# Performance work log

Measured on AMD Instinct MI355X. Metric: run time of the kernel, lower is better.

## Reference

```python
import jax, jax.numpy as jnp
import numpy as np

# --- Instant-NGP hashgrid config (from INGP.build_encoding) ---
L = 16            # cfg_model.encoding.levels
F = 2             # cfg_model.encoding.hashgrid.dim
T = 1 << 19       # 2 ** log2_hashmap_size
BASE = 16         # 2 ** min_logres
FINEST = 2048     # 2 ** max_logres
GROWTH = np.exp((np.log(FINEST) - np.log(BASE)) / (L - 1))
RES = np.floor(BASE * GROWTH ** np.arange(L)).astype(np.float32)  # per-level resolution
VMIN, VMAX = -1.0, 1.0  # voxel_range
N_POINTS = 524288

# 8 trilinear corner offsets, and NGP spatial-hash primes
CORNERS = np.array([[i, j, k] for i in (0, 1) for j in (0, 1) for k in (0, 1)],
                   dtype=np.uint32)                       # [8,3]
PRIMES = np.array([1, 2654435761, 805459861], dtype=np.uint32)


def setup_inputs() -> dict:
    key = jax.random.key(0)
    k1, k2 = jax.random.split(key)
    points_3D = jax.random.uniform(k1, (N_POINTS, 3), minval=-1.0, maxval=1.0,
                                   dtype=jnp.float32)
    # torch-ngp 'uniform' init: U(-1e-4, 1e-4)
    tables = jax.random.uniform(k2, (L, T, F), minval=-1e-4, maxval=1e-4,
                                dtype=jnp.float32)
    return {"points_3D": points_3D, "tables": tables}


def _hash_encode(x, tables):
    """x: [N,3] in [0,1]; tables: [L,T,F] -> [N, L*F]."""
    corners_u = jnp.asarray(CORNERS)            # [8,3] uint32
    corners_b = jnp.asarray(CORNERS.astype(bool))
    p0u, p1u, p2u = (jnp.uint32(int(p)) for p in PRIMES)
    mask = jnp.uint32(T - 1)

    def level(table, r):
        pos = x * r                              # [N,3]
        p0 = jnp.floor(pos)
        w = pos - p0                             # trilinear weights [N,3]
        c = p0.astype(jnp.uint32)[:, None, :] + corners_u[None]  # [N,8,3]
        h = (c[..., 0] * p0u) ^ (c[..., 1] * p1u) ^ (c[..., 2] * p2u)
        idx = (h & mask).astype(jnp.int32)       # [N,8] hashed bucket ids
        vals = table[idx]                        # [N,8,F] irregular gather
        wc = jnp.where(corners_b[None], w[:, None, :], 1.0 - w[:, None, :]).prod(-1)
        return jnp.einsum('nc,ncf->nf', wc, vals)  # [N,F]

    feats = jax.vmap(level)(tables, jnp.asarray(RES))  # [L,N,F]
    n = x.shape[0]
    return jnp.transpose(feats, (1, 0, 2)).reshape(n, L * F)


def reference(points_3D, tables):
    # _encode_3D with contract=False: normalize to [0,1] over voxel_range
    x = (points_3D - VMIN) / (VMAX - VMIN)
    feat = _hash_encode(x, tables)
    return feat.astype(jnp.float32)
```

## Files before the change

kernel.cpp:

```cpp
#include <hip/hip_runtime.h>
#include <cmath>


constexpr int LVLS = 16;
constexpr unsigned TBL = 1u << 19;
constexpr unsigned TMASK = TBL - 1u;
constexpr unsigned P1 = 2654435761u;
constexpr unsigned P2 = 805459861u;
constexpr int NBINS = 32768;
constexpr int CAP = 24;
constexpr int MAIN = NBINS * CAP;
constexpr int OVCAP = 65536;
constexpr int S_TOT = MAIN + OVCAP;
constexpr int SLOTS_PER_FINE_BLOCK = 512;

typedef float vf2 __attribute__((ext_vector_type(2)));
typedef float vf4 __attribute__((ext_vector_type(4)));

struct ResArr { float r[LVLS]; };

__device__ __forceinline__ unsigned spread5(unsigned v) {
    v &= 31u;
    v = (v | (v << 8)) & 0x100Fu;
    v = (v | (v << 4)) & 0x10C3u;
    v = (v | (v << 2)) & 0x1249u;
    return v;
}

__device__ __forceinline__ unsigned bin_key(float px, float py, float pz) {
    float x = (px + 1.0f) * 0.5f;
    float y = (py + 1.0f) * 0.5f;
    float z = (pz + 1.0f) * 0.5f;
    unsigned bx = (unsigned)fminf(31.f, fmaxf(0.f, floorf(x * 32.f)));
    unsigned by = (unsigned)fminf(31.f, fmaxf(0.f, floorf(y * 32.f)));
    unsigned bz = (unsigned)fminf(31.f, fmaxf(0.f, floorf(z * 32.f)));
    return spread5(bx) | (spread5(by) << 1) | (spread5(bz) << 2);
}

__device__ __forceinline__ void level_gather(
    const float2* __restrict__ tab, float r,
    float x, float y, float z, float& f0, float& f1)
{
    float posx = x * r, posy = y * r, posz = z * r;
    float fx = floorf(posx), fy = floorf(posy), fz = floorf(posz);
    float wx = posx - fx, wy = posy - fy, wz = posz - fz;
    unsigned ix = (unsigned)fx, iy = (unsigned)fy, iz = (unsigned)fz;
    unsigned hx0 = ix, hx1 = ix + 1u;
    unsigned hy0 = iy * P1;
    unsigned hz0 = iz * P2, hz1 = hz0 + P2;

    unsigned hyz[4];
    hyz[0] = hy0 ^ hz0;
    hyz[1] = hy0 ^ hz1;
    hyz[2] = (hy0 + P1) ^ hz0;
    hyz[3] = (hy0 + P1) ^ hz1;

    float2 v[8];
    if ((ix & 1u) == 0u) {
        #pragma unroll
        for (int yz = 0; yz < 4; ++yz) {
            unsigned b0 = (hx0 ^ hyz[yz]) & TMASK;
            vf4 qd = *(const vf4*)(tab + (b0 & ~1u));
            float2 lo = make_float2(qd.x, qd.y);
            float2 hi = make_float2(qd.z, qd.w);
            bool odd = (b0 & 1u) != 0u;
            v[yz]     = odd ? hi : lo;
            v[4 + yz] = odd ? lo : hi;
        }
    } else {
        #pragma unroll
        for (int yz = 0; yz < 4; ++yz) {
            unsigned b0 = (hx0 ^ hyz[yz]) & TMASK;
            unsigned b1 = (hx1 ^ hyz[yz]) & TMASK;
            v[yz]     = tab[b0];
            v[4 + yz] = tab[b1];
        }
    }

    float ox = 1.0f - wx, oy = 1.0f - wy, oz = 1.0f - wz;
    float w[8];
    w[0] = (ox * oy) * oz;
    w[1] = (ox * oy) * wz;
    w[2] = (ox * wy) * oz;
    w[3] = (ox * wy) * wz;
    w[4] = (wx * oy) * oz;
    w[5] = (wx * oy) * wz;
    w[6] = (wx * wy) * oz;
    w[7] = (wx * wy) * wz;

    f0 = w[0] * v[0].x;
    f1 = w[0] * v[0].y;
    #pragma unroll
    for (int c = 1; c < 8; ++c) {
        f0 += w[c] * v[c].x;
        f1 += w[c] * v[c].y;
    }
}

__device__ __forceinline__ void encode_point_direct(
    const float* __restrict__ tables, const ResArr& ra,
    float px, float py, float pz, vf4* __restrict__ row)
{
    float x = (px + 1.0f) * 0.5f;
    float y = (py + 1.0f) * 0.5f;
    float z = (pz + 1.0f) * 0.5f;
    float acc[2 * LVLS];
    #pragma unroll
    for (int l = 0; l < LVLS; ++l) {
        const float2* __restrict__ tab = (const float2*)tables + (size_t)l * TBL;
        float f0, f1;
        level_gather(tab, ra.r[l], x, y, z, f0, f1);
        acc[2 * l] = f0; acc[2 * l + 1] = f1;
    }
    #pragma unroll
    for (int k = 0; k < 8; ++k) {
        vf4 o;
        o.x = acc[4 * k + 0]; o.y = acc[4 * k + 1];
        o.z = acc[4 * k + 2]; o.w = acc[4 * k + 3];
        __builtin_nontemporal_store(o, row + k);
    }
}

__global__ __launch_bounds__(256) void ingp_scatter1(
    const float* __restrict__ pts, unsigned* __restrict__ cnt,
    vf4* __restrict__ slots, const float* __restrict__ tables,
    vf4* __restrict__ out, ResArr ra, int npts)
{
    int i = blockIdx.x * 256 + threadIdx.x;
    if (i >= npts) return;
    float px = pts[i * 3 + 0], py = pts[i * 3 + 1], pz = pts[i * 3 + 2];
    unsigned bin = bin_key(px, py, pz);
    unsigned pos = atomicAdd(&cnt[bin], 1u);
    vf4 o; o.x = px; o.y = py; o.z = pz; o.w = __int_as_float(i);
    if (pos < (unsigned)CAP) {
        __builtin_nontemporal_store(o, slots + (size_t)bin * CAP + pos);
    } else {
        unsigned ov = atomicAdd(&cnt[NBINS], 1u);
        if (ov < (unsigned)OVCAP) {
            __builtin_nontemporal_store(o, slots + MAIN + ov);
        } else {
            encode_point_direct(tables, ra, px, py, pz,
                                out + (size_t)i * 8);
        }
    }
}

__device__ __forceinline__ bool slot_valid(
    const unsigned* __restrict__ cnt, int sidx)
{
    if (sidx < MAIN) {
        unsigned bin = (unsigned)sidx / (unsigned)CAP;
        unsigned within = (unsigned)sidx - bin * (unsigned)CAP;
        unsigned c = cnt[bin];
        return within < (c < (unsigned)CAP ? c : (unsigned)CAP);
    } else {
        unsigned idx = (unsigned)(sidx - MAIN);
        unsigned c = cnt[NBINS];
        return idx < (c < (unsigned)OVCAP ? c : (unsigned)OVCAP);
    }
}

__global__ __launch_bounds__(256) void ingp_fine(
    const vf4* __restrict__ slots, const unsigned* __restrict__ cnt,
    const float* __restrict__ tables,
    float2* __restrict__ ws,
    ResArr ra)
{
    int b = blockIdx.x;
    int lvl = 8 + (b & 7);
    int q = b >> 3;
    int t = threadIdx.x;

    float r = ra.r[lvl];
    const float2* __restrict__ tab = (const float2*)tables + (size_t)lvl * TBL;
    float2* __restrict__ wrow = ws + (size_t)(lvl - 8) * S_TOT;

    #pragma unroll
    for (int s = 0; s < 2; ++s) {
        int sidx = q * SLOTS_PER_FINE_BLOCK + t + s * 256;
        if (!slot_valid(cnt, sidx)) continue;
        vf4 v = slots[sidx];
        float x = (v.x + 1.0f) * 0.5f;
        float y = (v.y + 1.0f) * 0.5f;
        float z = (v.z + 1.0f) * 0.5f;
        float f0, f1;
        level_gather(tab, r, x, y, z, f0, f1);
        vf2 o; o.x = f0; o.y = f1;
        __builtin_nontemporal_store(o, (vf2*)(wrow + sidx));
    }
}

__global__ __launch_bounds__(256) void ingp_finish(
    const vf4* __restrict__ slots, const unsigned* __restrict__ cnt,
    const float* __restrict__ tables,
    const float2* __restrict__ ws,
    vf4* __restrict__ out,
    ResArr ra)
{
    __shared__ float2 a[LVLS][258];
    __shared__ int s_orig[256];
    int base = blockIdx.x * 256;
    int t = threadIdx.x;
    int sidx = base + t;

    bool valid = slot_valid(cnt, sidx);
    float px = -1.0f, py = -1.0f, pz = -1.0f;
    int orig = -1;
    if (valid) {
        vf4 v4 = slots[sidx];
        px = v4.x; py = v4.y; pz = v4.z;
        orig = __float_as_int(v4.w);
    }
    s_orig[t] = orig;
    float x = (px + 1.0f) * 0.5f;
    float y = (py + 1.0f) * 0.5f;
    float z = (pz + 1.0f) * 0.5f;

    #pragma unroll
    for (int l = 0; l < 8; ++l) {
        const float2* __restrict__ tab = (const float2*)tables + (size_t)l * TBL;
        float f0, f1;
        level_gather(tab, ra.r[l], x, y, z, f0, f1);
        a[l][t] = make_float2(f0, f1);
    }
    #pragma unroll
    for (int l = 8; l < LVLS; ++l) {
        vf2 w = __builtin_nontemporal_load(
            (const vf2*)(ws + (size_t)(l - 8) * S_TOT + sidx));
        a[l][t] = make_float2(w.x, w.y);
    }
    __syncthreads();

    int j = t & 7;
    int pl = t >> 3;
    #pragma unroll
    for (int it = 0; it < 8; ++it) {
        int pt = pl + it * 32;
        int og = s_orig[pt];
        if (og >= 0) {
            float2 u = a[2 * j][pt];
            float2 v = a[2 * j + 1][pt];
            vf4 o; o.x = u.x; o.y = u.y; o.z = v.x; o.w = v.y;
            __builtin_nontemporal_store(o, (vf4*)(out + (size_t)og * 8 + j));
        }
    }
}

__global__ __launch_bounds__(256) void ingp_fused_raw(
    const float* __restrict__ pts,
    const float* __restrict__ tables,
    vf4* __restrict__ out, ResArr ra, int npts)
{
    int i = blockIdx.x * 256 + threadIdx.x;
    if (i >= npts) return;
    encode_point_direct(tables, ra,
                        pts[i * 3 + 0], pts[i * 3 + 1], pts[i * 3 + 2],
                        out + (size_t)i * 8);
}

extern "C" void kernel_launch(void* const* d_in, const int* in_sizes, int n_in,
                              void* d_out, int out_size, void* d_ws, size_t ws_size,
                              hipStream_t stream) {
    const float* pts    = (const float*)d_in[0];
    const float* tables = (const float*)d_in[1];
    int npts = in_sizes[0] / 3;

    ResArr ra;
    double growth = exp((log(2048.0) - log(16.0)) / 15.0);
    for (int l = 0; l < LVLS; ++l)
        ra.r[l] = (float)floor(16.0 * pow(growth, (double)l));

    int pgrid = (npts + 255) / 256;

    size_t fine_bytes = 8ull * S_TOT * sizeof(float2);
    size_t slot_bytes = (size_t)S_TOT * sizeof(vf4);
    size_t cnt_bytes  = (NBINS + 1) * sizeof(unsigned);
    size_t need = fine_bytes + slot_bytes + cnt_bytes;

    if (ws_size >= need) {
        char* w = (char*)d_ws;
        float2*   wsf   = (float2*)w;        w += fine_bytes;
        vf4*      slots = (vf4*)w;           w += slot_bytes;
        unsigned* cnt   = (unsigned*)w;

        hipMemsetAsync(cnt, 0, cnt_bytes, stream);
        hipLaunchKernelGGL(ingp_scatter1, dim3(pgrid), dim3(256), 0, stream,
                           pts, cnt, slots, tables, (vf4*)d_out, ra, npts);
        hipLaunchKernelGGL(ingp_fine,
                           dim3(8 * (S_TOT / SLOTS_PER_FINE_BLOCK)), dim3(256),
                           0, stream, slots, cnt, tables, wsf, ra);
        hipLaunchKernelGGL(ingp_finish, dim3(S_TOT / 256), dim3(256), 0, stream,
                           slots, cnt, tables, wsf, (vf4*)d_out, ra);
    } else {
        hipLaunchKernelGGL(ingp_fused_raw, dim3(pgrid), dim3(256), 0, stream,
                           pts, tables, (vf4*)d_out, ra, npts);
    }
}
```

Before: 309.3 us.

## Fold coarse-level gathers into the fine kernel and slim the finish pass

Moves the coarse levels 0-7 gather work out of the finish kernel and into the fine-level kernel. Every fifth group of blocks handles coarse levels for 256 slots and writes output features 0-15 directly, so coarse and fine gathers run concurrently in one launch. The finish kernel now only copies the eight fine-level results from the workspace into output columns 16-31. Bin capacity drops from 24 to 20 to shrink the slot array, at the risk of more overflow into the shared overflow region. Slot reads now use nontemporal loads.

Result: slower. 348.1 us (+12.5%).

```diff
diff --git a/kernel.cpp b/kernel.cpp
--- a/kernel.cpp
+++ b/kernel.cpp
@@ -8,11 +8,13 @@
 constexpr unsigned P1 = 2654435761u;
 constexpr unsigned P2 = 805459861u;
 constexpr int NBINS = 32768;
-constexpr int CAP = 24;
+constexpr int CAP = 20;
 constexpr int MAIN = NBINS * CAP;
 constexpr int OVCAP = 65536;
 constexpr int S_TOT = MAIN + OVCAP;
-constexpr int SLOTS_PER_FINE_BLOCK = 512;
+constexpr int NFINE = S_TOT / 512;
+constexpr int NCOARSE = S_TOT / 256;
+constexpr int T_OCT = NFINE + NCOARSE / 8;
 
 typedef float vf2 __attribute__((ext_vector_type(2)));
 typedef float vf4 __attribute__((ext_vector_type(4)));
@@ -160,88 +162,115 @@
     }
 }
 
-__global__ __launch_bounds__(256) void ingp_fine(
+__global__ __launch_bounds__(256) void ingp_fuse(
     const vf4* __restrict__ slots, const unsigned* __restrict__ cnt,
     const float* __restrict__ tables,
     float2* __restrict__ ws,
+    vf4* __restrict__ out,
     ResArr ra)
 {
+    __shared__ float2 a[8][258];
+    __shared__ int s_orig[256];
     int b = blockIdx.x;
-    int lvl = 8 + (b & 7);
-    int q = b >> 3;
+    int oct = b >> 3, l8 = b & 7;
     int t = threadIdx.x;
 
-    float r = ra.r[lvl];
-    const float2* __restrict__ tab = (const float2*)tables + (size_t)lvl * TBL;
-    float2* __restrict__ wrow = ws + (size_t)(lvl - 8) * S_TOT;
-
-    #pragma unroll
-    for (int s = 0; s < 2; ++s) {
-        int sidx = q * SLOTS_PER_FINE_BLOCK + t + s * 256;
-        if (!slot_valid(cnt, sidx)) continue;
-        vf4 v = slots[sidx];
-        float x = (v.x + 1.0f) * 0.5f;
-        float y = (v.y + 1.0f) * 0.5f;
-        float z = (v.z + 1.0f) * 0.5f;
-        float f0, f1;
-        level_gather(tab, r, x, y, z, f0, f1);
-        vf2 o; o.x = f0; o.y = f1;
-        __builtin_nontemporal_store(o, (vf2*)(wrow + sidx));
+    if (oct % 5 == 4) {
+        int c = (oct / 5) * 8 + l8;
+        int sidx = c * 256 + t;
+        bool valid = slot_valid(cnt, sidx);
+        float px = -1.0f, py = -1.0f, pz = -1.0f;
+        int orig = -1;
+        if (valid) {
+            vf4 v = __builtin_nontemporal_load(slots + sidx);
+            px = v.x; py = v.y; pz = v.z; orig = __float_as_int(v.w);
+        }
+        s_orig[t] = orig;
+        float x = (px + 1.0f) * 0.5f;
+        float y = (py + 1.0f) * 0.5f;
+        float z = (pz + 1.0f) * 0.5f;
+        #pragma unroll
+        for (int l = 0; l < 8; ++l) {
+            const float2* __restrict__ tab =
+                (const float2*)tables + (size_t)l * TBL;
+            float f0, f1;
+            level_gather(tab, ra.r[l], x, y, z, f0, f1);
+            a[l][t] = make_float2(f0, f1);
+        }
+        __syncthreads();
+        int j = t & 3, sl = t >> 2;
+        #pragma unroll
+        for (int it = 0; it < 4; ++it) {
+            int s = sl + it * 64;
+            int og = s_orig[s];
+            if (og >= 0) {
+                float2 u = a[2 * j][s];
+                float2 v = a[2 * j + 1][s];
+                vf4 o; o.x = u.x; o.y = u.y; o.z = v.x; o.w = v.y;
+                __builtin_nontemporal_store(o, out + (size_t)og * 8 + j);
+            }
+        }
+    } else {
+        int f = (oct / 5) * 4 + (oct % 5);
+        int lvl = 8 + l8;
+        float r = ra.r[lvl];
+        const float2* __restrict__ tab =
+            (const float2*)tables + (size_t)lvl * TBL;
+        float2* __restrict__ wrow = ws + (size_t)l8 * S_TOT;
+
+        #pragma unroll
+        for (int s = 0; s < 2; ++s) {
+            int sidx = f * 512 + t + s * 256;
+            if (!slot_valid(cnt, sidx)) continue;
+            vf4 v = __builtin_nontemporal_load(slots + sidx);
+            float x = (v.x + 1.0f) * 0.5f;
+            float y = (v.y + 1.0f) * 0.5f;
+            float z = (v.z + 1.0f) * 0.5f;
+            float f0, f1;
+            level_gather(tab, r, x, y, z, f0, f1);
+            vf2 o; o.x = f0; o.y = f1;
+            __builtin_nontemporal_store(o, (vf2*)(wrow + sidx));
+        }
     }
 }
 
 __global__ __launch_bounds__(256) void ingp_finish(
     const vf4* __restrict__ slots, const unsigned* __restrict__ cnt,
-    const float* __restrict__ tables,
     const float2* __restrict__ ws,
-    vf4* __restrict__ out,
-    ResArr ra)
-{
-    __shared__ float2 a[LVLS][258];
+    vf4* __restrict__ out)
+{
+    __shared__ float2 a[8][258];
     __shared__ int s_orig[256];
     int base = blockIdx.x * 256;
     int t = threadIdx.x;
     int sidx = base + t;
 
     bool valid = slot_valid(cnt, sidx);
-    float px = -1.0f, py = -1.0f, pz = -1.0f;
     int orig = -1;
     if (valid) {
-        vf4 v4 = slots[sidx];
-        px = v4.x; py = v4.y; pz = v4.z;
-        orig = __float_as_int(v4.w);
+        vf4 v = __builtin_nontemporal_load(slots + sidx);
+        orig = __float_as_int(v.w);
     }
     s_orig[t] = orig;
-    float x = (px + 1.0f) * 0.5f;
-    float y = (py + 1.0f) * 0.5f;
-    float z = (pz + 1.0f) * 0.5f;
 
     #pragma unroll
     for (int l = 0; l < 8; ++l) {
-        const float2* __restrict__ tab = (const float2*)tables + (size_t)l * TBL;
-        float f0, f1;
-        level_gather(tab, ra.r[l], x, y, z, f0, f1);
-        a[l][t] = make_float2(f0, f1);
-    }
-    #pragma unroll
-    for (int l = 8; l < LVLS; ++l) {
         vf2 w = __builtin_nontemporal_load(
-            (const vf2*)(ws + (size_t)(l - 8) * S_TOT + sidx));
+            (const vf2*)(ws + (size_t)l * S_TOT + sidx));
         a[l][t] = make_float2(w.x, w.y);
     }
     __syncthreads();
 
-    int j = t & 7;
-    int pl = t >> 3;
-    #pragma unroll
-    for (int it = 0; it < 8; ++it) {
-        int pt = pl + it * 32;
-        int og = s_orig[pt];
+    int j = t & 3, sl = t >> 2;
+    #pragma unroll
+    for (int it = 0; it < 4; ++it) {
+        int s = sl + it * 64;
+        int og = s_orig[s];
         if (og >= 0) {
-            float2 u = a[2 * j][pt];
-            float2 v = a[2 * j + 1][pt];
+            float2 u = a[2 * j][s];
+            float2 v = a[2 * j + 1][s];
             vf4 o; o.x = u.x; o.y = u.y; o.z = v.x; o.w = v.y;
-            __builtin_nontemporal_store(o, (vf4*)(out + (size_t)og * 8 + j));
+            __builtin_nontemporal_store(o, out + (size_t)og * 8 + 4 + j);
         }
     }
 }
@@ -286,11 +315,10 @@
         hipMemsetAsync(cnt, 0, cnt_bytes, stream);
         hipLaunchKernelGGL(ingp_scatter1, dim3(pgrid), dim3(256), 0, stream,
                            pts, cnt, slots, tables, (vf4*)d_out, ra, npts);
-        hipLaunchKernelGGL(ingp_fine,
-                           dim3(8 * (S_TOT / SLOTS_PER_FINE_BLOCK)), dim3(256),
-                           0, stream, slots, cnt, tables, wsf, ra);
+        hipLaunchKernelGGL(ingp_fuse, dim3(T_OCT * 8), dim3(256), 0, stream,
+                           slots, cnt, tables, wsf, (vf4*)d_out, ra);
         hipLaunchKernelGGL(ingp_finish, dim3(S_TOT / 256), dim3(256), 0, stream,
-                           slots, cnt, tables, wsf, (vf4*)d_out, ra);
+                           slots, cnt, wsf, (vf4*)d_out);
     } else {
         hipLaunchKernelGGL(ingp_fused_raw, dim3(pgrid), dim3(256), 0, stream,
                            pts, tables, (vf4*)d_out, ra, npts);
```
